# Kernel tuning notes

Hardware: AMD Instinct MI355X
Metric: run time of the kernel (lower is better)

Reference implementation:

```python
import jax, jax.numpy as jnp
import numpy as np

EPS = 1e-5
NEG_SLOPE = 0.01
GROUPS = 8


def leaky(x):
    return jnp.where(x >= 0, x, NEG_SLOPE * x)


def group_norm(x, gamma, beta):
    # torchsparse GroupNorm on a single-batch sparse tensor: normalize over
    # all points and the channels within each group. x: [N, C]
    N, C = x.shape
    xg = x.reshape(N, GROUPS, C // GROUPS)
    mean = xg.mean(axis=(0, 2), keepdims=True)
    var = xg.var(axis=(0, 2), keepdims=True)
    xn = ((xg - mean) * jax.lax.rsqrt(var + EPS)).reshape(N, C)
    return xn * gamma + beta


def spconv(feats, W, in_map, out_map, n_out):
    # Rulebook gather -> per-offset GEMM -> scatter-add.
    # feats: [N_in, Cin], W: [K, Cin, Cout], in_map/out_map: [K, M]
    Cout = W.shape[-1]
    g = feats[in_map]                               # [K, M, Cin] gather
    c = jnp.einsum('kmc,kcd->kmd', g, W)            # [K, M, Cout]
    out = jnp.zeros((n_out, Cout), feats.dtype)
    return out.at[out_map.reshape(-1)].add(c.reshape(-1, Cout))


def residual_block(h, Wa, ga, ba, Wb, gb, bb, m_in, m_out, n_out):
    y = group_norm(spconv(h, Wa, m_in, m_out, n_out), ga, ba)
    y = group_norm(spconv(y, Wb, m_in, m_out, n_out), gb, bb)
    return leaky(y + h)  # identity downsample (inc==outc, stride==1)


def setup_inputs() -> dict:
    key = jax.random.key(0)
    ks = jax.random.split(key, 12)
    N_in, N_out, C = 600000, 150000, 64
    M1, M2 = 75000, 60000
    sc = 0.05
    inp = {
        'x': jax.random.normal(ks[0], (N_in, C), jnp.float32),
        'W1': jax.random.normal(ks[1], (8, C, C), jnp.float32) * sc,
        'g1': jnp.ones((C,), jnp.float32), 'b1': jnp.zeros((C,), jnp.float32),
        'Wa1': jax.random.normal(ks[2], (27, C, C), jnp.float32) * sc,
        'ga1': jnp.ones((C,), jnp.float32), 'ba1': jnp.zeros((C,), jnp.float32),
        'Wb1': jax.random.normal(ks[3], (27, C, C), jnp.float32) * sc,
        'gb1': jnp.ones((C,), jnp.float32), 'bb1': jnp.zeros((C,), jnp.float32),
        'Wa2': jax.random.normal(ks[4], (27, C, C), jnp.float32) * sc,
        'ga2': jnp.ones((C,), jnp.float32), 'ba2': jnp.zeros((C,), jnp.float32),
        'Wb2': jax.random.normal(ks[5], (27, C, C), jnp.float32) * sc,
        'gb2': jnp.ones((C,), jnp.float32), 'bb2': jnp.zeros((C,), jnp.float32),
        'm1_in': jax.random.randint(ks[6], (8, M1), 0, N_in, jnp.int32),
        'm1_out': jax.random.randint(ks[7], (8, M1), 0, N_out, jnp.int32),
        'm2_in': jax.random.randint(ks[8], (27, M2), 0, N_out, jnp.int32),
        'm2_out': jax.random.randint(ks[9], (27, M2), 0, N_out, jnp.int32),
        'n_out': N_out,
    }
    return inp


def reference(x, W1, g1, b1, Wa1, ga1, ba1, Wb1, gb1, bb1,
              Wa2, ga2, ba2, Wb2, gb2, bb2,
              m1_in, m1_out, m2_in, m2_out, n_out):
    # BasicConvolutionBlock: Conv3d(ks=2, stride=2) -> GroupNorm(8) -> LeakyReLU
    h = leaky(group_norm(spconv(x, W1, m1_in, m1_out, n_out), g1, b1))
    # ResidualBlock x2: (Conv3d ks=3 -> GN -> Conv3d ks=3 -> GN) + identity, LeakyReLU
    h = residual_block(h, Wa1, ga1, ba1, Wb1, gb1, bb1, m2_in, m2_out, n_out)
    h = residual_block(h, Wa2, ga2, ba2, Wb2, gb2, bb2, m2_in, m2_out, n_out)
    return h
```

## Files before the change

### kernel.cpp

```cpp
#include <hip/hip_runtime.h>

#define NEG_SLOPE 0.01f
#define GN_EPS 1e-5f

typedef __attribute__((ext_vector_type(8))) __bf16 bf16x8;
typedef __attribute__((ext_vector_type(4))) __bf16 bf16x4;
typedef __attribute__((ext_vector_type(4))) float f32x4;
typedef __attribute__((ext_vector_type(2))) unsigned uintx2;

__device__ __forceinline__ float bf_lo(unsigned v) { return __uint_as_float(v << 16); }
__device__ __forceinline__ float bf_hi(unsigned v) { return __uint_as_float(v & 0xffff0000u); }

__global__ __launch_bounds__(256) void hist_kernel(
    const int* __restrict__ om, int* __restrict__ cnt, int E)
{
    const int stride = gridDim.x * blockDim.x;
    for (int e = blockIdx.x * blockDim.x + threadIdx.x; e < E; e += stride)
        atomicAdd(&cnt[om[e]], 1);
}

__global__ __launch_bounds__(256) void scan1_kernel(
    const int* __restrict__ cnt, int* __restrict__ part, int N)
{
    __shared__ int ls[256];
    int b = blockIdx.x, t = threadIdx.x;
    int i0 = b * 1024 + t * 4, s = 0;
#pragma unroll
    for (int u = 0; u < 4; ++u) if (i0 + u < N) s += cnt[i0 + u];
    ls[t] = s; __syncthreads();
    for (int off = 128; off > 0; off >>= 1) {
        if (t < off) ls[t] += ls[t + off];
        __syncthreads();
    }
    if (t == 0) part[b] = ls[0];
}

__global__ void scan2_kernel(int* __restrict__ part, int nb)
{
    if (blockIdx.x == 0 && threadIdx.x == 0) {
        int run = 0;
        for (int i = 0; i < nb; ++i) { int v = part[i]; part[i] = run; run += v; }
    }
}

__global__ __launch_bounds__(256) void scan3_kernel(
    const int* __restrict__ cnt, const int* __restrict__ part,
    int* __restrict__ base, int N)
{
    __shared__ int ls[256];
    int b = blockIdx.x, t = threadIdx.x;
    int i0 = b * 1024 + t * 4;
    int v0 = 0, v1 = 0, v2 = 0, v3 = 0;
    if (i0 + 0 < N) v0 = cnt[i0 + 0];
    if (i0 + 1 < N) v1 = cnt[i0 + 1];
    if (i0 + 2 < N) v2 = cnt[i0 + 2];
    if (i0 + 3 < N) v3 = cnt[i0 + 3];
    int s = v0 + v1 + v2 + v3;
    ls[t] = s; __syncthreads();
    for (int off = 1; off < 256; off <<= 1) {
        int x = (t >= off) ? ls[t - off] : 0;
        __syncthreads();
        ls[t] += x;
        __syncthreads();
    }
    int run = part[b] + ls[t] - s;
    if (i0 + 0 < N) { base[i0 + 0] = run; run += v0; if (i0 + 0 == N - 1) base[N] = run; }
    if (i0 + 1 < N) { base[i0 + 1] = run; run += v1; if (i0 + 1 == N - 1) base[N] = run; }
    if (i0 + 2 < N) { base[i0 + 2] = run; run += v2; if (i0 + 2 == N - 1) base[N] = run; }
    if (i0 + 3 < N) { base[i0 + 3] = run; run += v3; if (i0 + 3 == N - 1) base[N] = run; }
}

__global__ __launch_bounds__(256) void scatter_kernel(
    const int* __restrict__ om, const int* __restrict__ base,
    int* __restrict__ cur, int* __restrict__ inv, int E)
{
    const int stride = gridDim.x * blockDim.x;
    for (int e = blockIdx.x * blockDim.x + threadIdx.x; e < E; e += stride) {
        int o = om[e];
        int p = base[o] + atomicAdd(&cur[o], 1);
        inv[e] = p;
    }
}

template<int F32IN, int NORM>
__global__ __launch_bounds__(256) void conv_mfma_kernel(
    const void* __restrict__ feats, const float* __restrict__ W,
    const int* __restrict__ in_map, const int* __restrict__ inv,
    __bf16* __restrict__ C, int M, int BPK,
    const float* __restrict__ stats, const float* __restrict__ gamma,
    const float* __restrict__ beta, float invc)
{
    const int lane = threadIdx.x & 63;
    const int wv   = threadIdx.x >> 6;
    const int k    = blockIdx.x / BPK;
    const int blk  = blockIdx.x % BPK;
    const int l15  = lane & 15;
    const int lg   = lane >> 4;

    float scv[2][8], shv[2][8];
    if (NORM) {
#pragma unroll
        for (int hh = 0; hh < 2; ++hh) {
            int g = hh * 4 + lg;
            float mean = stats[g] * invc;
            float var  = fmaf(-mean, mean, stats[8 + g] * invc);
            float rstd = rsqrtf(var + GN_EPS);
#pragma unroll
            for (int j = 0; j < 8; ++j) {
                int ch = hh * 32 + lg * 8 + j;
                float s = rstd * gamma[ch];
                scv[hh][j] = s;
                shv[hh][j] = fmaf(-mean, s, beta[ch]);
            }
        }
    }

    const float* Wk = W + (size_t)k * 4096;
    bf16x8 b[4][2];
#pragma unroll
    for (int nt = 0; nt < 4; ++nt)
#pragma unroll
        for (int h = 0; h < 2; ++h)
#pragma unroll
            for (int j = 0; j < 8; ++j)
                b[nt][h][j] = (__bf16)Wk[(h * 32 + lg * 8 + j) * 64 + nt * 16 + l15];

    const int* imk   = in_map + (size_t)k * M;
    const int ntiles = (M + 15) >> 4;
    const int wpk    = BPK * 4;

    for (int t = blk * 4 + wv; t < ntiles; t += wpk) {
        int m  = t * 16 + l15;
        int mc = m < M ? m : M - 1;
        int ii = imk[mc];
        bf16x8 a0, a1;
        if (F32IN) {
            const float4* rp = (const float4*)((const float*)feats + (size_t)ii * 64 + lg * 8);
            float4 u0 = rp[0], u1 = rp[1];
            float4 u2 = rp[8], u3 = rp[9];
            float lo[8] = {u0.x, u0.y, u0.z, u0.w, u1.x, u1.y, u1.z, u1.w};
            float hi[8] = {u2.x, u2.y, u2.z, u2.w, u3.x, u3.y, u3.z, u3.w};
#pragma unroll
            for (int j = 0; j < 8; ++j) {
                float v0 = lo[j], v1 = hi[j];
                if (NORM) {
                    v0 = fmaf(v0, scv[0][j], shv[0][j]);
                    v1 = fmaf(v1, scv[1][j], shv[1][j]);
                }
                a0[j] = (__bf16)v0;
                a1[j] = (__bf16)v1;
            }
        } else {
            const bf16x8* rp = (const bf16x8*)((const __bf16*)feats + (size_t)ii * 64 + lg * 8);
            a0 = rp[0];
            a1 = rp[4];
        }
        f32x4 c0 = {0.f,0.f,0.f,0.f}, c1 = c0, c2 = c0, c3 = c0;
        c0 = __builtin_amdgcn_mfma_f32_16x16x32_bf16(a0, b[0][0], c0, 0, 0, 0);
        c1 = __builtin_amdgcn_mfma_f32_16x16x32_bf16(a0, b[1][0], c1, 0, 0, 0);
        c2 = __builtin_amdgcn_mfma_f32_16x16x32_bf16(a0, b[2][0], c2, 0, 0, 0);
        c3 = __builtin_amdgcn_mfma_f32_16x16x32_bf16(a0, b[3][0], c3, 0, 0, 0);
        c0 = __builtin_amdgcn_mfma_f32_16x16x32_bf16(a1, b[0][1], c0, 0, 0, 0);
        c1 = __builtin_amdgcn_mfma_f32_16x16x32_bf16(a1, b[1][1], c1, 0, 0, 0);
        c2 = __builtin_amdgcn_mfma_f32_16x16x32_bf16(a1, b[2][1], c2, 0, 0, 0);
        c3 = __builtin_amdgcn_mfma_f32_16x16x32_bf16(a1, b[3][1], c3, 0, 0, 0);

        const int e_base = k * M + t * 16;
        f32x4 cc[4] = {c0, c1, c2, c3};
#pragma unroll
        for (int r = 0; r < 4; ++r) {
            int row = lg * 4 + r;
            if (t * 16 + row < M) {
                int p = inv[e_base + row];
                __bf16* cr = C + (size_t)p * 64 + l15;
#pragma unroll
                for (int nt = 0; nt < 4; ++nt) {
                    __bf16 v = (__bf16)cc[nt][r];
                    __builtin_nontemporal_store(v, cr + nt * 16);
                }
            }
        }
    }
}

__global__ __launch_bounds__(256) void reduce_kernel(
    const unsigned* __restrict__ C2, const int* __restrict__ base,
    float* __restrict__ out, float* __restrict__ stats, int N)
{
    const int lane = threadIdx.x & 63;
    const int wv   = threadIdx.x >> 6;
    const int rq   = lane >> 4;
    const int cq   = lane & 15;
    float rs = 0.f, rqsum = 0.f;

    const int ostride = gridDim.x * 4;
    for (int o = blockIdx.x * 4 + wv; o < N; o += ostride) {
        const int s = base[o], t = base[o + 1];
        float a0 = 0.f, a1 = 0.f, a2 = 0.f, a3 = 0.f;
        for (int i = s + rq; i < t; i += 4) {
            uintx2 v = __builtin_nontemporal_load(
                (const uintx2*)(C2 + (size_t)i * 32 + cq * 2));
            a0 += bf_lo(v.x); a1 += bf_hi(v.x);
            a2 += bf_lo(v.y); a3 += bf_hi(v.y);
        }
        a0 += __shfl_xor(a0, 16); a1 += __shfl_xor(a1, 16);
        a2 += __shfl_xor(a2, 16); a3 += __shfl_xor(a3, 16);
        a0 += __shfl_xor(a0, 32); a1 += __shfl_xor(a1, 32);
        a2 += __shfl_xor(a2, 32); a3 += __shfl_xor(a3, 32);
        if (rq == 0) {
            float4 r = {a0, a1, a2, a3};
            *(float4*)(out + (size_t)o * 64 + cq * 4) = r;
            rs    += (a0 + a1) + (a2 + a3);
            rqsum += (a0 * a0 + a1 * a1) + (a2 * a2 + a3 * a3);
        }
    }
    rs += __shfl_xor(rs, 1); rqsum += __shfl_xor(rqsum, 1);
    __shared__ float ls[4][16];
    if (rq == 0 && (cq & 1) == 0) {
        ls[wv][cq >> 1] = rs;
        ls[wv][8 + (cq >> 1)] = rqsum;
    }
    __syncthreads();
    if (threadIdx.x < 16) {
        float t = (ls[0][threadIdx.x] + ls[1][threadIdx.x]) +
                  (ls[2][threadIdx.x] + ls[3][threadIdx.x]);
        unsafeAtomicAdd(stats + threadIdx.x, t);
    }
}

__global__ __launch_bounds__(256) void conv_kernel(
    const float* __restrict__ feats, const float* __restrict__ W,
    const int* __restrict__ in_map, const int* __restrict__ out_map,
    float* __restrict__ out, int M, int BPK)
{
    const int lane = threadIdx.x & 63;
    const int wv   = threadIdx.x >> 6;
    const int k    = blockIdx.x / BPK;
    const int blk  = blockIdx.x % BPK;
    const float* Wk = W + (size_t)k * 4096;
    float w[64];
#pragma unroll
    for (int c = 0; c < 64; ++c) w[c] = Wk[c * 64 + lane];
    __shared__ float fbuf[4][64];
    const int* im = in_map + (size_t)k * M;
    const int* om = out_map + (size_t)k * M;
    const int stride = BPK * 4;
    for (int m = blk * 4 + wv; m < M; m += stride) {
        int ii = im[m];
        int oi = om[m];
        float f = feats[(size_t)ii * 64 + lane];
        fbuf[wv][lane] = f;
        const float* fb = fbuf[wv];
        float a0 = 0.f, a1 = 0.f, a2 = 0.f, a3 = 0.f;
#pragma unroll
        for (int c = 0; c < 64; c += 4) {
            float4 f4 = *(const float4*)(fb + c);
            a0 = fmaf(f4.x, w[c + 0], a0);
            a1 = fmaf(f4.y, w[c + 1], a1);
            a2 = fmaf(f4.z, w[c + 2], a2);
            a3 = fmaf(f4.w, w[c + 3], a3);
        }
        unsafeAtomicAdd(out + (size_t)oi * 64 + lane, (a0 + a1) + (a2 + a3));
    }
}

__global__ __launch_bounds__(256) void gn_stats_kernel(
    const float4* __restrict__ x, float* __restrict__ stats, long total4)
{
    const int lane = threadIdx.x & 63;
    float s = 0.f, q = 0.f;
    const long stride = (long)gridDim.x * blockDim.x;
    for (long i = (long)blockIdx.x * blockDim.x + threadIdx.x; i < total4; i += stride) {
        float4 v = x[i];
        s += (v.x + v.y) + (v.z + v.w);
        q += (v.x * v.x + v.y * v.y) + (v.z * v.z + v.w * v.w);
    }
    s += __shfl_xor(s, 1);  q += __shfl_xor(q, 1);
    s += __shfl_xor(s, 16); q += __shfl_xor(q, 16);
    s += __shfl_xor(s, 32); q += __shfl_xor(q, 32);
    __shared__ float ls[4][16];
    const int wv = threadIdx.x >> 6;
    const int g = (lane >> 1) & 7;
    if (lane < 16 && (lane & 1) == 0) { ls[wv][g] = s; ls[wv][8 + g] = q; }
    __syncthreads();
    if (threadIdx.x < 16) {
        float t = (ls[0][threadIdx.x] + ls[1][threadIdx.x]) +
                  (ls[2][threadIdx.x] + ls[3][threadIdx.x]);
        unsafeAtomicAdd(stats + threadIdx.x, t);
    }
}

__global__ __launch_bounds__(256) void gn_apply_kernel(
    const float4* __restrict__ x, const float* __restrict__ stats,
    const float* __restrict__ gamma, const float* __restrict__ beta,
    const float4* resid, float4* out_f, bf16x4* out_bf,
    long total4, float invc, int do_leaky)
{
    __shared__ float sc[64], sh[64];
    if (threadIdx.x < 64) {
        int c = threadIdx.x, g = c >> 3;
        float mean = stats[g] * invc;
        float var  = fmaf(-mean, mean, stats[8 + g] * invc);
        float s    = rsqrtf(var + GN_EPS) * gamma[c];
        sc[c] = s;
        sh[c] = fmaf(-mean, s, beta[c]);
    }
    __syncthreads();
    const long stride = (long)gridDim.x * blockDim.x;
    for (long i = (long)blockIdx.x * blockDim.x + threadIdx.x; i < total4; i += stride) {
        float4 v = x[i];
        int c0 = ((int)(i & 15)) << 2;
        float4 r;
        r.x = fmaf(v.x, sc[c0 + 0], sh[c0 + 0]);
        r.y = fmaf(v.y, sc[c0 + 1], sh[c0 + 1]);
        r.z = fmaf(v.z, sc[c0 + 2], sh[c0 + 2]);
        r.w = fmaf(v.w, sc[c0 + 3], sh[c0 + 3]);
        if (resid) {
            float4 h4 = resid[i];
            r.x += h4.x; r.y += h4.y; r.z += h4.z; r.w += h4.w;
        }
        if (do_leaky) {
            r.x = r.x >= 0.f ? r.x : NEG_SLOPE * r.x;
            r.y = r.y >= 0.f ? r.y : NEG_SLOPE * r.y;
            r.z = r.z >= 0.f ? r.z : NEG_SLOPE * r.z;
            r.w = r.w >= 0.f ? r.w : NEG_SLOPE * r.w;
        }
        if (out_f) out_f[i] = r;
        if (out_bf) {
            bf16x4 o;
            o.x = (__bf16)r.x; o.y = (__bf16)r.y; o.z = (__bf16)r.z; o.w = (__bf16)r.w;
            out_bf[i] = o;
        }
    }
}

extern "C" void kernel_launch(void* const* d_in, const int* in_sizes, int n_in,
                              void* d_out, int out_size, void* d_ws, size_t ws_size,
                              hipStream_t stream) {
    const float* x   = (const float*)d_in[0];
    const float* W1  = (const float*)d_in[1];
    const float* g1  = (const float*)d_in[2];
    const float* b1  = (const float*)d_in[3];
    const float* Wa1 = (const float*)d_in[4];
    const float* ga1 = (const float*)d_in[5];
    const float* ba1 = (const float*)d_in[6];
    const float* Wb1 = (const float*)d_in[7];
    const float* gb1 = (const float*)d_in[8];
    const float* bb1 = (const float*)d_in[9];
    const float* Wa2 = (const float*)d_in[10];
    const float* ga2 = (const float*)d_in[11];
    const float* ba2 = (const float*)d_in[12];
    const float* Wb2 = (const float*)d_in[13];
    const float* gb2 = (const float*)d_in[14];
    const float* bb2 = (const float*)d_in[15];
    const int* m1_in  = (const int*)d_in[16];
    const int* m1_out = (const int*)d_in[17];
    const int* m2_in  = (const int*)d_in[18];
    const int* m2_out = (const int*)d_in[19];

    const int N   = out_size / 64;
    const int M1  = in_sizes[16] / 8;
    const int M2  = in_sizes[18] / 27;
    const int E1  = 8 * M1;
    const int E2  = 27 * M2;
    const int Emax = E1 > E2 ? E1 : E2;

    float* h = (float*)d_out;
    const long  total4 = (long)N * 16;
    const float invc   = 1.f / ((float)N * 8.f);

    char* wp = (char*)d_ws;
    size_t off = 0;
    auto alloc = [&](size_t bytes) {
        void* p = wp + off;
        off = (off + bytes + 255) & ~(size_t)255;
        return p;
    };
    float*  accA  = (float*)alloc((size_t)N * 64 * 4);
    float*  accB  = (float*)alloc((size_t)N * 64 * 4);
    __bf16* hbf   = (__bf16*)alloc((size_t)N * 64 * 2);
    __bf16* Cbuf  = (__bf16*)alloc((size_t)Emax * 64 * 2);
    int*    base1 = (int*)alloc((size_t)(N + 1) * 4);
    int*    base2 = (int*)alloc((size_t)(N + 1) * 4);
    int*    cnt   = (int*)alloc((size_t)N * 4);
    int*    part  = (int*)alloc(4096);
    int*    inv1  = (int*)alloc((size_t)E1 * 4);
    int*    inv2  = (int*)alloc((size_t)E2 * 4);
    float*  stats = (float*)alloc(5 * 16 * 4);
    const size_t need = off;

    if (ws_size < need) {
        float* y  = accB;
        float* st = stats;
        const size_t nbytes = (size_t)N * 64 * 4;
        auto convL = [&](const float* feats, const float* W, const int* im,
                         const int* om, int K, int M, int BPK) {
            hipMemsetAsync(accA, 0, nbytes, stream);
            conv_kernel<<<dim3(K * BPK), 256, 0, stream>>>(feats, W, im, om, accA, M, BPK);
        };
        auto gnL = [&](const float* gamma, const float* beta, const float* resid,
                       float* outp, int leaky) {
            hipMemsetAsync(st, 0, 16 * sizeof(float), stream);
            gn_stats_kernel<<<1024, 256, 0, stream>>>((const float4*)accA, st, total4);
            gn_apply_kernel<<<1024, 256, 0, stream>>>((const float4*)accA, st, gamma, beta,
                                                      (const float4*)resid, (float4*)outp,
                                                      nullptr, total4, invc, leaky);
        };
        convL(x, W1, m1_in, m1_out, 8, M1, 320); gnL(g1, b1, nullptr, h, 1);
        convL(h, Wa1, m2_in, m2_out, 27, M2, 96); gnL(ga1, ba1, nullptr, y, 0);
        convL(y, Wb1, m2_in, m2_out, 27, M2, 96); gnL(gb1, bb1, h, h, 1);
        convL(h, Wa2, m2_in, m2_out, 27, M2, 96); gnL(ga2, ba2, nullptr, y, 0);
        convL(y, Wb2, m2_in, m2_out, 27, M2, 96); gnL(gb2, bb2, h, h, 1);
        return;
    }

    hipMemsetAsync(stats, 0, 5 * 16 * sizeof(float), stream);

    const int nb = (N + 1023) / 1024;
    auto buildCSR = [&](const int* om, int E, int* base, int* inv) {
        hipMemsetAsync(cnt, 0, (size_t)N * 4, stream);
        hist_kernel<<<2048, 256, 0, stream>>>(om, cnt, E);
        scan1_kernel<<<nb, 256, 0, stream>>>(cnt, part, N);
        scan2_kernel<<<1, 64, 0, stream>>>(part, nb);
        scan3_kernel<<<nb, 256, 0, stream>>>(cnt, part, base, N);
        hipMemsetAsync(cnt, 0, (size_t)N * 4, stream);
        scatter_kernel<<<2048, 256, 0, stream>>>(om, base, cnt, inv, E);
    };
    buildCSR(m1_out, E1, base1, inv1);
    buildCSR(m2_out, E2, base2, inv2);

    float* st0  = stats;
    float* stA1 = stats + 16;
    float* stB1 = stats + 32;
    float* stA2 = stats + 48;
    float* stB2 = stats + 64;

    auto conv = [&](const void* feats, int variant, const float* W, const int* im,
                    int K, int M, int BPK, const int* base, const int* inv,
                    float* accOut, float* statOut,
                    const float* nstats, const float* ngamma, const float* nbeta) {
        dim3 grid(K * BPK);
        if (variant == 2)
            conv_mfma_kernel<1, 1><<<grid, 256, 0, stream>>>(feats, W, im, inv, Cbuf,
                M, BPK, nstats, ngamma, nbeta, invc);
        else if (variant == 1)
            conv_mfma_kernel<1, 0><<<grid, 256, 0, stream>>>(feats, W, im, inv, Cbuf,
                M, BPK, nullptr, nullptr, nullptr, invc);
        else
            conv_mfma_kernel<0, 0><<<grid, 256, 0, stream>>>(feats, W, im, inv, Cbuf,
                M, BPK, nullptr, nullptr, nullptr, invc);
        reduce_kernel<<<2048, 256, 0, stream>>>((const unsigned*)Cbuf, base,
                                                accOut, statOut, N);
    };
    auto gn = [&](const float* src, const float* st, const float* gamma,
                  const float* beta, const float* resid, float* outf,
                  __bf16* outbf, int leaky) {
        gn_apply_kernel<<<1024, 256, 0, stream>>>((const float4*)src, st, gamma, beta,
                                                  (const float4*)resid, (float4*)outf,
                                                  (bf16x4*)outbf, total4, invc, leaky);
    };

    conv(x, 1, W1, m1_in, 8, M1, 128, base1, inv1, accA, st0, nullptr, nullptr, nullptr);
    gn(accA, st0, g1, b1, nullptr, h, hbf, 1);
    conv(hbf, 0, Wa1, m2_in, 27, M2, 64, base2, inv2, accA, stA1, nullptr, nullptr, nullptr);
    conv(accA, 2, Wb1, m2_in, 27, M2, 64, base2, inv2, accB, stB1, stA1, ga1, ba1);
    gn(accB, stB1, gb1, bb1, h, h, hbf, 1);
    conv(hbf, 0, Wa2, m2_in, 27, M2, 64, base2, inv2, accA, stA2, nullptr, nullptr, nullptr);
    conv(accA, 2, Wb2, m2_in, 27, M2, 64, base2, inv2, accB, stB2, stA2, ga2, ba2);
    gn(accB, stB2, gb2, bb2, h, h, nullptr, 1);
}
```

Baseline: 1.174 ms.

## Materialize normalized intermediate as bf16 instead of fusing GN into conv gather

Drops the fused GroupNorm-on-gather path for the second conv of each residual block. It adds an explicit gn_apply pass that writes the normalized activations as a bf16 buffer, and the next conv then gathers bf16 rows (half the bytes of fp32) instead of fp32 rows plus per-element FMA. Separately, it merges the two fp32 accumulators into one, reuses Cbuf as scratch in the fallback path, and changes blocks-per-offset counts. The trade is one extra elementwise kernel launch and pass over N×64 per block in exchange for a lighter, more cache-friendly gather across 27×60k rows.

```diff
diff --git a/kernel.cpp b/kernel.cpp
--- a/kernel.cpp
+++ b/kernel.cpp
@@ -82,13 +82,11 @@
     }
 }
 
-template<int F32IN, int NORM>
+template<int F32IN>
 __global__ __launch_bounds__(256) void conv_mfma_kernel(
     const void* __restrict__ feats, const float* __restrict__ W,
     const int* __restrict__ in_map, const int* __restrict__ inv,
-    __bf16* __restrict__ C, int M, int BPK,
-    const float* __restrict__ stats, const float* __restrict__ gamma,
-    const float* __restrict__ beta, float invc)
+    __bf16* __restrict__ C, int M, int BPK)
 {
     const int lane = threadIdx.x & 63;
     const int wv   = threadIdx.x >> 6;
@@ -96,24 +94,6 @@
     const int blk  = blockIdx.x % BPK;
     const int l15  = lane & 15;
     const int lg   = lane >> 4;
-
-    float scv[2][8], shv[2][8];
-    if (NORM) {
-#pragma unroll
-        for (int hh = 0; hh < 2; ++hh) {
-            int g = hh * 4 + lg;
-            float mean = stats[g] * invc;
-            float var  = fmaf(-mean, mean, stats[8 + g] * invc);
-            float rstd = rsqrtf(var + GN_EPS);
-#pragma unroll
-            for (int j = 0; j < 8; ++j) {
-                int ch = hh * 32 + lg * 8 + j;
-                float s = rstd * gamma[ch];
-                scv[hh][j] = s;
-                shv[hh][j] = fmaf(-mean, s, beta[ch]);
-            }
-        }
-    }
 
     const float* Wk = W + (size_t)k * 4096;
     bf16x8 b[4][2];
@@ -138,18 +118,10 @@
             const float4* rp = (const float4*)((const float*)feats + (size_t)ii * 64 + lg * 8);
             float4 u0 = rp[0], u1 = rp[1];
             float4 u2 = rp[8], u3 = rp[9];
-            float lo[8] = {u0.x, u0.y, u0.z, u0.w, u1.x, u1.y, u1.z, u1.w};
-            float hi[8] = {u2.x, u2.y, u2.z, u2.w, u3.x, u3.y, u3.z, u3.w};
-#pragma unroll
-            for (int j = 0; j < 8; ++j) {
-                float v0 = lo[j], v1 = hi[j];
-                if (NORM) {
-                    v0 = fmaf(v0, scv[0][j], shv[0][j]);
-                    v1 = fmaf(v1, scv[1][j], shv[1][j]);
-                }
-                a0[j] = (__bf16)v0;
-                a1[j] = (__bf16)v1;
-            }
+            a0[0] = (__bf16)u0.x; a0[1] = (__bf16)u0.y; a0[2] = (__bf16)u0.z; a0[3] = (__bf16)u0.w;
+            a0[4] = (__bf16)u1.x; a0[5] = (__bf16)u1.y; a0[6] = (__bf16)u1.z; a0[7] = (__bf16)u1.w;
+            a1[0] = (__bf16)u2.x; a1[1] = (__bf16)u2.y; a1[2] = (__bf16)u2.z; a1[3] = (__bf16)u2.w;
+            a1[4] = (__bf16)u3.x; a1[5] = (__bf16)u3.y; a1[6] = (__bf16)u3.z; a1[7] = (__bf16)u3.w;
         } else {
             const bf16x8* rp = (const bf16x8*)((const __bf16*)feats + (size_t)ii * 64 + lg * 8);
             a0 = rp[0];
@@ -376,9 +348,9 @@
         off = (off + bytes + 255) & ~(size_t)255;
         return p;
     };
-    float*  accA  = (float*)alloc((size_t)N * 64 * 4);
-    float*  accB  = (float*)alloc((size_t)N * 64 * 4);
+    float*  acc   = (float*)alloc((size_t)N * 64 * 4);
     __bf16* hbf   = (__bf16*)alloc((size_t)N * 64 * 2);
+    __bf16* ybf   = (__bf16*)alloc((size_t)N * 64 * 2);
     __bf16* Cbuf  = (__bf16*)alloc((size_t)Emax * 64 * 2);
     int*    base1 = (int*)alloc((size_t)(N + 1) * 4);
     int*    base2 = (int*)alloc((size_t)(N + 1) * 4);
@@ -390,19 +362,19 @@
     const size_t need = off;
 
     if (ws_size < need) {
-        float* y  = accB;
+        float* y  = (float*)Cbuf;
         float* st = stats;
         const size_t nbytes = (size_t)N * 64 * 4;
         auto convL = [&](const float* feats, const float* W, const int* im,
                          const int* om, int K, int M, int BPK) {
-            hipMemsetAsync(accA, 0, nbytes, stream);
-            conv_kernel<<<dim3(K * BPK), 256, 0, stream>>>(feats, W, im, om, accA, M, BPK);
+            hipMemsetAsync(acc, 0, nbytes, stream);
+            conv_kernel<<<dim3(K * BPK), 256, 0, stream>>>(feats, W, im, om, acc, M, BPK);
         };
         auto gnL = [&](const float* gamma, const float* beta, const float* resid,
                        float* outp, int leaky) {
             hipMemsetAsync(st, 0, 16 * sizeof(float), stream);
-            gn_stats_kernel<<<1024, 256, 0, stream>>>((const float4*)accA, st, total4);
-            gn_apply_kernel<<<1024, 256, 0, stream>>>((const float4*)accA, st, gamma, beta,
+            gn_stats_kernel<<<1024, 256, 0, stream>>>((const float4*)acc, st, total4);
+            gn_apply_kernel<<<1024, 256, 0, stream>>>((const float4*)acc, st, gamma, beta,
                                                       (const float4*)resid, (float4*)outp,
                                                       nullptr, total4, invc, leaky);
         };
@@ -435,37 +407,32 @@
     float* stA2 = stats + 48;
     float* stB2 = stats + 64;
 
-    auto conv = [&](const void* feats, int variant, const float* W, const int* im,
+    auto conv = [&](const void* feats, int f32in, const float* W, const int* im,
                     int K, int M, int BPK, const int* base, const int* inv,
-                    float* accOut, float* statOut,
-                    const float* nstats, const float* ngamma, const float* nbeta) {
+                    float* statOut) {
         dim3 grid(K * BPK);
-        if (variant == 2)
-            conv_mfma_kernel<1, 1><<<grid, 256, 0, stream>>>(feats, W, im, inv, Cbuf,
-                M, BPK, nstats, ngamma, nbeta, invc);
-        else if (variant == 1)
-            conv_mfma_kernel<1, 0><<<grid, 256, 0, stream>>>(feats, W, im, inv, Cbuf,
-                M, BPK, nullptr, nullptr, nullptr, invc);
+        if (f32in)
+            conv_mfma_kernel<1><<<grid, 256, 0, stream>>>(feats, W, im, inv, Cbuf, M, BPK);
         else
-            conv_mfma_kernel<0, 0><<<grid, 256, 0, stream>>>(feats, W, im, inv, Cbuf,
-                M, BPK, nullptr, nullptr, nullptr, invc);
+            conv_mfma_kernel<0><<<grid, 256, 0, stream>>>(feats, W, im, inv, Cbuf, M, BPK);
         reduce_kernel<<<2048, 256, 0, stream>>>((const unsigned*)Cbuf, base,
-                                                accOut, statOut, N);
+                                                acc, statOut, N);
     };
-    auto gn = [&](const float* src, const float* st, const float* gamma,
-                  const float* beta, const float* resid, float* outf,
-                  __bf16* outbf, int leaky) {
-        gn_apply_kernel<<<1024, 256, 0, stream>>>((const float4*)src, st, gamma, beta,
+    auto gn = [&](const float* st, const float* gamma, const float* beta,
+                  const float* resid, float* outf, __bf16* outbf, int leaky) {
+        gn_apply_kernel<<<1024, 256, 0, stream>>>((const float4*)acc, st, gamma, beta,
                                                   (const float4*)resid, (float4*)outf,
                                                   (bf16x4*)outbf, total4, invc, leaky);
     };
 
-    conv(x, 1, W1, m1_in, 8, M1, 128, base1, inv1, accA, st0, nullptr, nullptr, nullptr);
-    gn(accA, st0, g1, b1, nullptr, h, hbf, 1);
-    conv(hbf, 0, Wa1, m2_in, 27, M2, 64, base2, inv2, accA, stA1, nullptr, nullptr, nullptr);
-    conv(accA, 2, Wb1, m2_in, 27, M2, 64, base2, inv2, accB, stB1, stA1, ga1, ba1);
-    gn(accB, stB1, gb1, bb1, h, h, hbf, 1);
-    conv(hbf, 0, Wa2, m2_in, 27, M2, 64, base2, inv2, accA, stA2, nullptr, nullptr, nullptr);
-    conv(accA, 2, Wb2, m2_in, 27, M2, 64, base2, inv2, accB, stB2, stA2, ga2, ba2);
-    gn(accB, stB2, gb2, bb2, h, h, nullptr, 1);
-}
+    conv(x, 1, W1, m1_in, 8, M1, 256, base1, inv1, st0);
+    gn(st0, g1, b1, nullptr, h, hbf, 1);
+    conv(hbf, 0, Wa1, m2_in, 27, M2, 96, base2, inv2, stA1);
+    gn(stA1, ga1, ba1, nullptr, nullptr, ybf, 0);
+    conv(ybf, 0, Wb1, m2_in, 27, M2, 96, base2, inv2, stB1);
+    gn(stB1, gb1, bb1, h, h, hbf, 1);
+    conv(hbf, 0, Wa2, m2_in, 27, M2, 96, base2, inv2, stA2);
+    gn(stA2, ga2, ba2, nullptr, nullptr, ybf, 0);
+    conv(ybf, 0, Wb2, m2_in, 27, M2, 96, base2, inv2, stB2);
+    gn(stB2, gb2, bb2, h, h, nullptr, 1);
+}
```

After: 1.078 ms. 8.1% less time.
